# Kernel optimization log

Hardware: AMD Instinct MI355X
Metric: run time of the kernel (lower is better)

The kernel has to match this reference:

```python
import jax, jax.numpy as jnp
import numpy as np

M, N, D = 8192, 8192, 256
GAMMA = 1.0 / D  # RBF bandwidth


def setup_inputs() -> dict:
    key = jax.random.key(0)
    k1, k2, k3 = jax.random.split(key, 3)
    Xq = jax.random.normal(k1, (M, D), dtype=jnp.float32)
    Xtrain = jax.random.normal(k2, (N, D), dtype=jnp.float32)
    alpha = jax.random.normal(k3, (N, 1), dtype=jnp.float32)
    return {"Xq": Xq, "Xtrain": Xtrain, "alpha": alpha}


def rbf_kernel(A, B):
    # squared euclidean distances via ||a||^2 + ||b||^2 - 2 a.b  -> [M, N]
    sq_a = jnp.sum(A * A, axis=1, keepdims=True)          # [M,1]
    sq_b = jnp.sum(B * B, axis=1, keepdims=True).T        # [1,N]
    d2 = sq_a + sq_b - 2.0 * jnp.einsum('md,nd->mn', A, B)
    d2 = jnp.maximum(d2, 0.0)
    return jnp.exp(-GAMMA * d2)


def reference(Xq, Xtrain, alpha):
    # forward: kernel(X, self.X) @ self.alpha  -> [M, 1]
    K = rbf_kernel(Xq, Xtrain)
    return K @ alpha
```

## Files before the change

kernel.cpp:

```cpp
#include <hip/hip_runtime.h>
#include <stdint.h>


#define MM 8192
#define NN 8192
#define DD 256
#define GAMMA (1.0f/256.0f)
#define LOG2E 1.44269504088896340736f
#define SCALE_A (2.0f*GAMMA*LOG2E)
#define NEG_G_LOG2E (-GAMMA*LOG2E)

#define NSPLIT 16
#define NPB (NN/NSPLIT)
#define NT_PER (NPB/16)

typedef __bf16 bf16x8 __attribute__((ext_vector_type(8)));
typedef float  f32x4  __attribute__((ext_vector_type(4)));

#define A_OFF  ((size_t)0)
#define B_OFF  ((size_t)4 << 20)
#define W_OFF  ((size_t)8 << 20)
#define EA_OFF (((size_t)8 << 20) + 32768)

__device__ __forceinline__ unsigned short f2bf(float f) {
  union { float f; uint32_t u; } x; x.f = f;
  uint32_t u = x.u;
  u += 0x7FFFu + ((u >> 16) & 1u);
  return (unsigned short)(u >> 16);
}
__device__ __forceinline__ uint32_t pack2(float a, float b) {
  return (uint32_t)f2bf(a) | ((uint32_t)f2bf(b) << 16);
}

__global__ __launch_bounds__(256) void prep_kernel(
    const float* __restrict__ Xq, const float* __restrict__ Xt,
    const float* __restrict__ alpha,
    char* __restrict__ Amat, char* __restrict__ Bmat,
    float* __restrict__ w, float* __restrict__ ea, float* __restrict__ out)
{
  const int gi = blockIdx.x * 256 + threadIdx.x;
  if (gi < MM) out[gi] = 0.f;

  const int lane = threadIdx.x & 63;
  const int gw = blockIdx.x * 4 + (threadIdx.x >> 6);
  const bool isA = gw < 512;
  const int t = isA ? gw : gw - 512;
  const float* __restrict__ src = isA ? Xq : Xt;
  char* __restrict__ dst = isA ? Amat : Bmat;
  const float sc = isA ? SCALE_A : 1.0f;
  const int n = t * 16 + (lane & 15);
  float ss = 0.f;
#pragma unroll
  for (int r = 0; r < 8; ++r) {
    const int gg = r * 4 + (lane >> 4);
    const float* p = src + (size_t)n * DD + gg * 8;
    const float4 f0 = *(const float4*)p;
    const float4 f1 = *(const float4*)(p + 4);
    ss += f0.x*f0.x + f0.y*f0.y + f0.z*f0.z + f0.w*f0.w
        + f1.x*f1.x + f1.y*f1.y + f1.z*f1.z + f1.w*f1.w;
    uint4 pk;
    pk.x = pack2(f0.x * sc, f0.y * sc); pk.y = pack2(f0.z * sc, f0.w * sc);
    pk.z = pack2(f1.x * sc, f1.y * sc); pk.w = pack2(f1.z * sc, f1.w * sc);
    *(uint4*)(dst + (size_t)t * 8192 + r * 1024 + lane * 16) = pk;
  }
  ss += __shfl_xor(ss, 16, 64);
  ss += __shfl_xor(ss, 32, 64);
  if (lane < 16) {
    if (isA) ea[n] = __builtin_amdgcn_exp2f(NEG_G_LOG2E * ss);
    else     w[n]  = alpha[n] * __builtin_amdgcn_exp2f(NEG_G_LOG2E * ss);
  }
}

__global__ __launch_bounds__(256, 2) void rbf_main(
    const char* __restrict__ Amat, const char* __restrict__ Bmat,
    const float* __restrict__ w, const float* __restrict__ ea,
    float* __restrict__ out)
{
  __shared__ float lds_w[NPB];
  const int tid  = threadIdx.x;
  const int wave = tid >> 6, lane = tid & 63;
  const int quad = lane >> 4, l16 = lane & 15;

  const int b    = blockIdx.x;
  const int xcd  = b & 7, slot = b >> 3;
  const int my   = (xcd & 3) * 8 + ((slot >> 5) << 2) + (slot & 3);
  const int nx   = (xcd >> 2) * 8 + ((slot >> 2) & 7);
  const int mt0    = my * 16 + wave * 4;
  const int nt0    = nx * NT_PER;
  const int nbase0 = nx * NPB;

  {
    const float2 wv2 = *(const float2*)(w + nbase0 + tid * 2);
    lds_w[tid * 2]     = wv2.x;
    lds_w[tid * 2 + 1] = wv2.y;
  }

  bf16x8 afrag[4][8];
#pragma unroll
  for (int rt = 0; rt < 4; ++rt)
#pragma unroll
    for (int kc = 0; kc < 8; ++kc) {
      union { uint4 u; bf16x8 v; } cv;
      cv.u = *(const uint4*)(Amat + (size_t)(mt0 + rt) * 8192 + kc * 1024 + lane * 16);
      afrag[rt][kc] = cv.v;
    }

  __syncthreads();

  float outacc[4][4] = {{0,0,0,0},{0,0,0,0},{0,0,0,0},{0,0,0,0}};

  uint4 bufA[8], bufB[8];
  auto loadB = [&](uint4* dst, int ct) {
#pragma unroll
    for (int kc = 0; kc < 8; ++kc)
      dst[kc] = *(const uint4*)(Bmat + (size_t)(nt0 + ct) * 8192 + kc * 1024 + lane * 16);
  };

  const f32x4 fzero = {0.f, 0.f, 0.f, 0.f};
  f32x4 accA[4], accB[4];

  auto mfmaInto = [&](f32x4* acc, const uint4* buf) {
#pragma unroll
    for (int rt = 0; rt < 4; ++rt) acc[rt] = fzero;
#pragma unroll
    for (int kc = 0; kc < 8; ++kc) {
      union { uint4 u; bf16x8 v; } cv; cv.u = buf[kc];
#pragma unroll
      for (int rt = 0; rt < 4; ++rt)
        acc[rt] = __builtin_amdgcn_mfma_f32_16x16x32_bf16(afrag[rt][kc], cv.v, acc[rt], 0, 0, 0);
    }
  };
  auto epi = [&](const f32x4* acc, int ct) {
    const float wv = lds_w[ct * 16 + l16];
#pragma unroll
    for (int rt = 0; rt < 4; ++rt) {
      outacc[rt][0] += wv * __builtin_amdgcn_exp2f(acc[rt][0]);
      outacc[rt][1] += wv * __builtin_amdgcn_exp2f(acc[rt][1]);
      outacc[rt][2] += wv * __builtin_amdgcn_exp2f(acc[rt][2]);
      outacc[rt][3] += wv * __builtin_amdgcn_exp2f(acc[rt][3]);
    }
  };

  loadB(bufA, 0);
  loadB(bufB, 1);
  mfmaInto(accA, bufA);
  for (int ct = 0; ct < NT_PER - 2; ct += 2) {
    loadB(bufA, ct + 2);
    mfmaInto(accB, bufB);
    epi(accA, ct);
    loadB(bufB, ct + 3);
    mfmaInto(accA, bufA);
    epi(accB, ct + 1);
  }
  mfmaInto(accB, bufB);
  epi(accA, NT_PER - 2);
  epi(accB, NT_PER - 1);

#pragma unroll
  for (int rt = 0; rt < 4; ++rt)
#pragma unroll
    for (int i = 0; i < 4; ++i) {
      float v = outacc[rt][i];
      v += __shfl_xor(v, 1, 64);
      v += __shfl_xor(v, 2, 64);
      v += __shfl_xor(v, 4, 64);
      v += __shfl_xor(v, 8, 64);
      if (l16 == 0) {
        const int row = my * 256 + wave * 64 + rt * 16 + quad * 4 + i;
        atomicAdd(&out[row], ea[row] * v);
      }
    }
}

extern "C" void kernel_launch(void* const* d_in, const int* in_sizes, int n_in,
                              void* d_out, int out_size, void* d_ws, size_t ws_size,
                              hipStream_t stream) {
  const float* Xq    = (const float*)d_in[0];
  const float* Xt    = (const float*)d_in[1];
  const float* alpha = (const float*)d_in[2];
  float* out = (float*)d_out;
  char*  ws  = (char*)d_ws;

  char*  Amat = ws + A_OFF;
  char*  Bmat = ws + B_OFF;
  float* w    = (float*)(ws + W_OFF);
  float* ea   = (float*)(ws + EA_OFF);

  hipLaunchKernelGGL(prep_kernel, dim3(256), dim3(256), 0, stream,
                     Xq, Xt, alpha, Amat, Bmat, w, ea, out);
  hipLaunchKernelGGL(rbf_main, dim3(512), dim3(256), 0, stream,
                     Amat, Bmat, w, ea, out);
}
```

Before: 103.6 us.

## Fuse Xq bf16 conversion and row norms into main RBF kernel

Drops the A-side prep in the prep kernel and has each main-kernel wave load Xq rows as fp32, compute the squared norms and pack the scaled bf16 A fragments directly in registers, storing exp(-gamma*||a||^2) in LDS. This removes a workspace round trip and halves the prep kernel's work. In exchange, every N-split block re-reads Xq in fp32 (16x redundancy, twice the bytes of bf16). The block-to-tile mapping is also changed.

```diff
diff --git a/kernel.cpp b/kernel.cpp
--- a/kernel.cpp
+++ b/kernel.cpp
@@ -17,10 +17,8 @@
 typedef __bf16 bf16x8 __attribute__((ext_vector_type(8)));
 typedef float  f32x4  __attribute__((ext_vector_type(4)));
 
-#define A_OFF  ((size_t)0)
-#define B_OFF  ((size_t)4 << 20)
-#define W_OFF  ((size_t)8 << 20)
-#define EA_OFF (((size_t)8 << 20) + 32768)
+#define B_OFF  ((size_t)0)
+#define W_OFF  ((size_t)4 << 20)
 
 __device__ __forceinline__ unsigned short f2bf(float f) {
   union { float f; uint32_t u; } x; x.f = f;
@@ -33,58 +31,48 @@
 }
 
 __global__ __launch_bounds__(256) void prep_kernel(
-    const float* __restrict__ Xq, const float* __restrict__ Xt,
-    const float* __restrict__ alpha,
-    char* __restrict__ Amat, char* __restrict__ Bmat,
-    float* __restrict__ w, float* __restrict__ ea, float* __restrict__ out)
+    const float* __restrict__ Xt, const float* __restrict__ alpha,
+    char* __restrict__ Bmat, float* __restrict__ w, float* __restrict__ out)
 {
   const int gi = blockIdx.x * 256 + threadIdx.x;
   if (gi < MM) out[gi] = 0.f;
 
   const int lane = threadIdx.x & 63;
-  const int gw = blockIdx.x * 4 + (threadIdx.x >> 6);
-  const bool isA = gw < 512;
-  const int t = isA ? gw : gw - 512;
-  const float* __restrict__ src = isA ? Xq : Xt;
-  char* __restrict__ dst = isA ? Amat : Bmat;
-  const float sc = isA ? SCALE_A : 1.0f;
+  const int t = blockIdx.x * 4 + (threadIdx.x >> 6);
   const int n = t * 16 + (lane & 15);
   float ss = 0.f;
 #pragma unroll
   for (int r = 0; r < 8; ++r) {
     const int gg = r * 4 + (lane >> 4);
-    const float* p = src + (size_t)n * DD + gg * 8;
+    const float* p = Xt + (size_t)n * DD + gg * 8;
     const float4 f0 = *(const float4*)p;
     const float4 f1 = *(const float4*)(p + 4);
     ss += f0.x*f0.x + f0.y*f0.y + f0.z*f0.z + f0.w*f0.w
         + f1.x*f1.x + f1.y*f1.y + f1.z*f1.z + f1.w*f1.w;
     uint4 pk;
-    pk.x = pack2(f0.x * sc, f0.y * sc); pk.y = pack2(f0.z * sc, f0.w * sc);
-    pk.z = pack2(f1.x * sc, f1.y * sc); pk.w = pack2(f1.z * sc, f1.w * sc);
-    *(uint4*)(dst + (size_t)t * 8192 + r * 1024 + lane * 16) = pk;
+    pk.x = pack2(f0.x, f0.y); pk.y = pack2(f0.z, f0.w);
+    pk.z = pack2(f1.x, f1.y); pk.w = pack2(f1.z, f1.w);
+    *(uint4*)(Bmat + (size_t)t * 8192 + r * 1024 + lane * 16) = pk;
   }
   ss += __shfl_xor(ss, 16, 64);
   ss += __shfl_xor(ss, 32, 64);
-  if (lane < 16) {
-    if (isA) ea[n] = __builtin_amdgcn_exp2f(NEG_G_LOG2E * ss);
-    else     w[n]  = alpha[n] * __builtin_amdgcn_exp2f(NEG_G_LOG2E * ss);
-  }
+  if (lane < 16) w[n] = alpha[n] * __builtin_amdgcn_exp2f(NEG_G_LOG2E * ss);
 }
 
 __global__ __launch_bounds__(256, 2) void rbf_main(
-    const char* __restrict__ Amat, const char* __restrict__ Bmat,
-    const float* __restrict__ w, const float* __restrict__ ea,
-    float* __restrict__ out)
+    const float* __restrict__ Xq, const char* __restrict__ Bmat,
+    const float* __restrict__ w, float* __restrict__ out)
 {
   __shared__ float lds_w[NPB];
+  __shared__ float lds_ea[4][64];
   const int tid  = threadIdx.x;
   const int wave = tid >> 6, lane = tid & 63;
   const int quad = lane >> 4, l16 = lane & 15;
 
   const int b    = blockIdx.x;
   const int xcd  = b & 7, slot = b >> 3;
-  const int my   = (xcd & 3) * 8 + ((slot >> 5) << 2) + (slot & 3);
-  const int nx   = (xcd >> 2) * 8 + ((slot >> 2) & 7);
+  const int my   = (xcd & 3) * 8 + (slot & 7);
+  const int nx   = (xcd >> 2) * 8 + (slot >> 3);
   const int mt0    = my * 16 + wave * 4;
   const int nt0    = nx * NT_PER;
   const int nbase0 = nx * NPB;
@@ -95,15 +83,34 @@
     lds_w[tid * 2 + 1] = wv2.y;
   }
 
+  float ssq[4] = {0.f, 0.f, 0.f, 0.f};
   bf16x8 afrag[4][8];
 #pragma unroll
-  for (int rt = 0; rt < 4; ++rt)
+  for (int rt = 0; rt < 4; ++rt) {
+    const float* rowp = Xq + (size_t)((mt0 + rt) * 16 + l16) * DD + quad * 8;
 #pragma unroll
     for (int kc = 0; kc < 8; ++kc) {
+      const float* p = rowp + kc * 32;
+      const float4 f0 = *(const float4*)p;
+      const float4 f1 = *(const float4*)(p + 4);
+      ssq[rt] += f0.x*f0.x + f0.y*f0.y + f0.z*f0.z + f0.w*f0.w
+               + f1.x*f1.x + f1.y*f1.y + f1.z*f1.z + f1.w*f1.w;
       union { uint4 u; bf16x8 v; } cv;
-      cv.u = *(const uint4*)(Amat + (size_t)(mt0 + rt) * 8192 + kc * 1024 + lane * 16);
+      cv.u.x = pack2(f0.x*SCALE_A, f0.y*SCALE_A);
+      cv.u.y = pack2(f0.z*SCALE_A, f0.w*SCALE_A);
+      cv.u.z = pack2(f1.x*SCALE_A, f1.y*SCALE_A);
+      cv.u.w = pack2(f1.z*SCALE_A, f1.w*SCALE_A);
       afrag[rt][kc] = cv.v;
     }
+  }
+#pragma unroll
+  for (int rt = 0; rt < 4; ++rt) {
+    float s = ssq[rt];
+    s += __shfl_xor(s, 16, 64);
+    s += __shfl_xor(s, 32, 64);
+    if (lane < 16)
+      lds_ea[wave][rt * 16 + lane] = __builtin_amdgcn_exp2f(NEG_G_LOG2E * s);
+  }
 
   __syncthreads();
 
@@ -167,7 +174,7 @@
       v += __shfl_xor(v, 8, 64);
       if (l16 == 0) {
         const int row = my * 256 + wave * 64 + rt * 16 + quad * 4 + i;
-        atomicAdd(&out[row], ea[row] * v);
+        atomicAdd(&out[row], lds_ea[wave][rt * 16 + quad * 4 + i] * v);
       }
     }
 }
@@ -181,13 +188,11 @@
   float* out = (float*)d_out;
   char*  ws  = (char*)d_ws;
 
-  char*  Amat = ws + A_OFF;
   char*  Bmat = ws + B_OFF;
   float* w    = (float*)(ws + W_OFF);
-  float* ea   = (float*)(ws + EA_OFF);
 
-  hipLaunchKernelGGL(prep_kernel, dim3(256), dim3(256), 0, stream,
-                     Xq, Xt, alpha, Amat, Bmat, w, ea, out);
+  hipLaunchKernelGGL(prep_kernel, dim3(128), dim3(256), 0, stream,
+                     Xt, alpha, Bmat, w, out);
   hipLaunchKernelGGL(rbf_main, dim3(512), dim3(256), 0, stream,
-                     Amat, Bmat, w, ea, out);
+                     Xq, Bmat, w, out);
 }
```

New measurement: 129.5 us. 25.0% more time.
